# Kernel optimization log

Hardware: AMD Instinct MI355X
Metric: run time of the kernel (lower is better)

## Reference

```python
import jax, jax.numpy as jnp
import numpy as np

N_NODES = 50000
N_EDGES = 800000
HIDDEN = 128
IN_DIM = 128
OUT_DIM = 1
N_LAYERS = 4
N_GRAPHS = 32
LN_EPS = 1e-5


def setup_inputs() -> dict:
    key = jax.random.key(0)
    ks = jax.random.split(key, 12)
    s = 1.0 / np.sqrt(HIDDEN)
    inp = {
        "x": jax.random.normal(ks[0], (N_NODES, IN_DIM), dtype=jnp.float32),
        "edge_index": jax.random.randint(ks[1], (2, N_EDGES), 0, N_NODES, dtype=jnp.int64),
        "batch": jnp.sort(jax.random.randint(ks[2], (N_NODES,), 0, N_GRAPHS, dtype=jnp.int64)),
        "W_emb": jax.random.normal(ks[3], (HIDDEN, IN_DIM), dtype=jnp.float32) * s,
        "b_emb": jax.random.normal(ks[4], (HIDDEN,), dtype=jnp.float32) * s,
        "W_layers": jax.random.normal(ks[5], (N_LAYERS, HIDDEN, HIDDEN), dtype=jnp.float32) * s,
        "b_layers": jax.random.normal(ks[6], (N_LAYERS, HIDDEN), dtype=jnp.float32) * s,
        "ln_gamma": 1.0 + 0.02 * jax.random.normal(ks[7], (N_LAYERS, HIDDEN), dtype=jnp.float32),
        "ln_beta": 0.02 * jax.random.normal(ks[8], (N_LAYERS, HIDDEN), dtype=jnp.float32),
        "W_out": jax.random.normal(ks[9], (OUT_DIM, HIDDEN), dtype=jnp.float32) * s,
    }
    return inp


def _layer_norm(x, gamma, beta):
    mu = jnp.mean(x, axis=-1, keepdims=True)
    var = jnp.mean(jnp.square(x - mu), axis=-1, keepdims=True)
    return (x - mu) * jax.lax.rsqrt(var + LN_EPS) * gamma + beta


def reference(x, edge_index, batch, W_emb, b_emb, W_layers, b_layers, ln_gamma, ln_beta, W_out):
    n = x.shape[0]
    # add self-loops (PyG GCNConv default)
    loop = jnp.arange(n, dtype=edge_index.dtype)
    row = jnp.concatenate([edge_index[0], loop])  # source nodes
    col = jnp.concatenate([edge_index[1], loop])  # target nodes
    # symmetric normalization: deg over targets
    deg = jax.ops.segment_sum(jnp.ones_like(col, dtype=x.dtype), col, num_segments=n)
    dis = jnp.where(deg > 0, jax.lax.rsqrt(jnp.maximum(deg, 1.0)), 0.0)
    norm = dis[row] * dis[col]  # [E+N]

    h = x @ W_emb.T + b_emb  # embedding layer
    for i in range(N_LAYERS):
        t = h @ W_layers[i].T                      # [N, H] linear first
        msg = t[row] * norm[:, None]               # gather + scale  [E+N, H]
        agg = jax.ops.segment_sum(msg, col, num_segments=n) + b_layers[i]
        h = _layer_norm(h + jax.nn.relu(agg), ln_gamma[i], ln_beta[i])

    out = h @ W_out.T                              # [N, OUT_DIM]
    sums = jax.ops.segment_sum(out, batch, num_segments=N_GRAPHS)
    cnts = jax.ops.segment_sum(jnp.ones((n,), out.dtype), batch, num_segments=N_GRAPHS)
    return sums / jnp.maximum(cnts, 1.0)[:, None]  # [N_GRAPHS, OUT_DIM]
```

## Files before the change

### kernel.cpp

```cpp
#include <hip/hip_runtime.h>
#include <hip/hip_fp16.h>

#define NN 50000
#define NE 800000
#define NH 128
#define NG 32
#define NL 4
#define NB 196
#define WSLOT (NH * NH)

typedef __attribute__((ext_vector_type(8))) short bf16x8;
typedef __attribute__((ext_vector_type(4))) float f32x4;
typedef __attribute__((ext_vector_type(2))) float f32x2;

__device__ inline short f2bf(float x) {
  union { float f; unsigned u; } v;
  v.f = x;
  unsigned r = v.u + 0x7FFF + ((v.u >> 16) & 1);
  return (short)(r >> 16);
}
__device__ inline float bf2f(short s) {
  union { unsigned u; float f; } v;
  v.u = ((unsigned)(unsigned short)s) << 16;
  return v.f;
}

__device__ inline int block_exscan(int v) {
  __shared__ int wsum[4];
  int tid = threadIdx.x, wave = tid >> 6, lane = tid & 63;
  int x = v;
#pragma unroll
  for (int off = 1; off < 64; off <<= 1) {
    int y = __shfl_up(x, off, 64);
    if (lane >= off) x += y;
  }
  if (lane == 63) wsum[wave] = x;
  __syncthreads();
  int wp = 0;
  if (wave > 0) wp += wsum[0];
  if (wave > 1) wp += wsum[1];
  if (wave > 2) wp += wsum[2];
  return wp + x - v;
}

__global__ __launch_bounds__(256) void prep_swizzle(const float* __restrict__ W_emb,
                                                    const float* __restrict__ W_layers,
                                                    short* __restrict__ hi,
                                                    short* __restrict__ lo) {
  int i = blockIdx.x * 256 + threadIdx.x;
  if (i >= 5 * WSLOT) return;
  int slot = i >> 14, f = i & (WSLOT - 1);
  int j = f & 7, lane = (f >> 3) & 63, tt = (f >> 9) & 7, ks = f >> 12;
  int n = tt * 16 + (lane & 15);
  int k = ks * 32 + ((lane >> 4) & 3) * 8 + j;
  const float* W = slot ? (W_layers + (size_t)(slot - 1) * WSLOT) : W_emb;
  float x = W[n * NH + k];
  short hh = f2bf(x);
  hi[i] = hh;
  lo[i] = f2bf(x - bf2f(hh));
}

__global__ __launch_bounds__(256) void hist_kernel(const int* __restrict__ col,
                                                   int* __restrict__ cnt,
                                                   int* __restrict__ rank) {
  int e = blockIdx.x * 256 + threadIdx.x;
  if (e < NE) rank[e] = atomicAdd(&cnt[col[e]], 1);
}

__global__ __launch_bounds__(256) void scan1_kernel(const int* __restrict__ cnt,
                                                    int* __restrict__ bsum,
                                                    float* __restrict__ dis) {
  int i = blockIdx.x * 256 + threadIdx.x;
  int v = (i < NN) ? cnt[i] : 0;
  if (i < NN) dis[i] = rsqrtf((float)(v + 1));
  int lane = threadIdx.x & 63;
  int s = v;
#pragma unroll
  for (int off = 32; off; off >>= 1) s += __shfl_down(s, off, 64);
  __shared__ int ws[4];
  if (lane == 0) ws[threadIdx.x >> 6] = s;
  __syncthreads();
  if (threadIdx.x == 0) bsum[blockIdx.x] = ws[0] + ws[1] + ws[2] + ws[3];
}

__global__ __launch_bounds__(256) void scan2_kernel(const int* __restrict__ bsum,
                                                    int* __restrict__ ebsum) {
  int tid = threadIdx.x;
  int v = (tid < NB) ? bsum[tid] : 0;
  int ex = block_exscan(v);
  if (tid < NB) ebsum[tid] = ex;
}

__global__ __launch_bounds__(256) void scan3_kernel(const int* __restrict__ cnt,
                                                    const int* __restrict__ ebsum,
                                                    int* __restrict__ offs) {
  int i = blockIdx.x * 256 + threadIdx.x;
  int v = (i < NN) ? cnt[i] : 0;
  int ex = block_exscan(v);
  if (i < NN) offs[i] = ebsum[blockIdx.x] + ex;
}

__global__ __launch_bounds__(256) void fill_kernel(const int* __restrict__ row,
                                                   const int* __restrict__ col,
                                                   const int* __restrict__ rank,
                                                   const float* __restrict__ dis,
                                                   const int* __restrict__ offs,
                                                   int2* __restrict__ csr) {
  int e = blockIdx.x * 256 + threadIdx.x;
  if (e < NE) {
    int d = col[e];
    int s = row[e];
    int pos = offs[d] + rank[e];
    csr[pos] = make_int2(s, __float_as_int(dis[s] * dis[d]));
  }
}

template <bool EMB, bool LAST>
__global__ __launch_bounds__(512) void gemm_mfma(const float* __restrict__ Xf,
                                                 const __half* __restrict__ Xh,
                                                 const short* __restrict__ Whi,
                                                 const short* __restrict__ Wlo,
                                                 const float* __restrict__ bias,
                                                 const __half* __restrict__ hprev,
                                                 const float* __restrict__ gamma,
                                                 const float* __restrict__ beta,
                                                 const float* __restrict__ Wout,
                                                 __half* __restrict__ hnew,
                                                 unsigned char* __restrict__ h8,
                                                 float* __restrict__ nodeval) {
  __shared__ short Wh[WSLOT];
  __shared__ short Wl[WSLOT];
  int tid = threadIdx.x;
#pragma unroll
  for (int i = tid * 8; i < WSLOT; i += 512 * 8) {
    *(bf16x8*)&Wh[i] = *(const bf16x8*)(Whi + i);
    *(bf16x8*)&Wl[i] = *(const bf16x8*)(Wlo + i);
  }
  __syncthreads();

  int wave = tid >> 6, lane = tid & 63;
  int quad = lane >> 4, r16 = lane & 15;
  int m0 = blockIdx.x * 128 + wave * 16;
  if (m0 >= NN) return;
  int mA = m0 + r16;

  f32x4 acc[8];
#pragma unroll
  for (int t = 0; t < 8; ++t) acc[t] = (f32x4){0.f, 0.f, 0.f, 0.f};

#pragma unroll
  for (int ks = 0; ks < 4; ++ks) {
    int klane = ks * 32 + quad * 8;
    float af[8];
    if (EMB) {
      const float* xr = Xf + (size_t)mA * NH + klane;
      float4 a0 = *(const float4*)xr;
      float4 a1 = *(const float4*)(xr + 4);
      af[0] = a0.x; af[1] = a0.y; af[2] = a0.z; af[3] = a0.w;
      af[4] = a1.x; af[5] = a1.y; af[6] = a1.z; af[7] = a1.w;
    } else {
      const __half2* xr = (const __half2*)(Xh + (size_t)mA * NH + klane);
#pragma unroll
      for (int q = 0; q < 4; ++q) {
        float2 f = __half22float2(xr[q]);
        af[2 * q] = f.x;
        af[2 * q + 1] = f.y;
      }
    }
    bf16x8 xhi, xlo;
#pragma unroll
    for (int j = 0; j < 8; ++j) {
      short h = f2bf(af[j]);
      xhi[j] = h;
      xlo[j] = f2bf(af[j] - bf2f(h));
    }
#pragma unroll
    for (int t = 0; t < 8; ++t) {
      int fidx = ((ks * 8 + t) * 64 + lane) << 3;
      bf16x8 whi = *(const bf16x8*)&Wh[fidx];
      bf16x8 wlo = *(const bf16x8*)&Wl[fidx];
      acc[t] = __builtin_amdgcn_mfma_f32_16x16x32_bf16(whi, xhi, acc[t], 0, 0, 0);
      acc[t] = __builtin_amdgcn_mfma_f32_16x16x32_bf16(whi, xlo, acc[t], 0, 0, 0);
      acc[t] = __builtin_amdgcn_mfma_f32_16x16x32_bf16(wlo, xhi, acc[t], 0, 0, 0);
    }
  }

  int m = m0 + r16;
  int cb = quad * 4;
  if (EMB) {
#pragma unroll
    for (int t = 0; t < 8; ++t) {
      int ch = t * 16 + cb;
      float4 bb = *(const float4*)(bias + ch);
      float o0 = acc[t][0] + bb.x, o1 = acc[t][1] + bb.y;
      float o2 = acc[t][2] + bb.z, o3 = acc[t][3] + bb.w;
      __half2 p01 = __float22half2_rn(make_float2(o0, o1));
      __half2 p23 = __float22half2_rn(make_float2(o2, o3));
      *(uint2*)(hnew + (size_t)m * NH + ch) =
          make_uint2(*(unsigned*)&p01, *(unsigned*)&p23);
      int v = 0;
      v = __builtin_amdgcn_cvt_pk_fp8_f32(o0, o1, v, 0);
      v = __builtin_amdgcn_cvt_pk_fp8_f32(o2, o3, v, 1);
      ((unsigned*)(h8 + (size_t)m * NH))[t * 4 + quad] = (unsigned)v;
    }
  } else {
    float v[8][4];
    float s = 0.f, s2 = 0.f;
#pragma unroll
    for (int t = 0; t < 8; ++t) {
      int ch = t * 16 + cb;
      float4 bb = *(const float4*)(bias + ch);
      uint2 hp = *(const uint2*)(hprev + (size_t)m * NH + ch);
      float2 h01 = __half22float2(*(__half2*)&hp.x);
      float2 h23 = __half22float2(*(__half2*)&hp.y);
      float hv[4] = {h01.x, h01.y, h23.x, h23.y};
      float bb4[4] = {bb.x, bb.y, bb.z, bb.w};
#pragma unroll
      for (int r = 0; r < 4; ++r) {
        float z = fmaxf(acc[t][r] + bb4[r], 0.f);
        float val = hv[r] + z;
        v[t][r] = val;
        s += val;
        s2 += val * val;
      }
    }
    s += __shfl_xor(s, 16, 64);
    s += __shfl_xor(s, 32, 64);
    s2 += __shfl_xor(s2, 16, 64);
    s2 += __shfl_xor(s2, 32, 64);
    float mean = s * (1.f / 128.f);
    float var = fmaxf(s2 * (1.f / 128.f) - mean * mean, 0.f);
    float inv = rsqrtf(var + 1e-5f);
    float d = 0.f;
#pragma unroll
    for (int t = 0; t < 8; ++t) {
      int ch = t * 16 + cb;
      float4 gv = *(const float4*)(gamma + ch);
      float4 bt = *(const float4*)(beta + ch);
      float o0 = (v[t][0] - mean) * inv * gv.x + bt.x;
      float o1 = (v[t][1] - mean) * inv * gv.y + bt.y;
      float o2 = (v[t][2] - mean) * inv * gv.z + bt.z;
      float o3 = (v[t][3] - mean) * inv * gv.w + bt.w;
      __half2 p01 = __float22half2_rn(make_float2(o0, o1));
      __half2 p23 = __float22half2_rn(make_float2(o2, o3));
      *(uint2*)(hnew + (size_t)m * NH + ch) =
          make_uint2(*(unsigned*)&p01, *(unsigned*)&p23);
      if (!LAST) {
        int pv = 0;
        pv = __builtin_amdgcn_cvt_pk_fp8_f32(o0, o1, pv, 0);
        pv = __builtin_amdgcn_cvt_pk_fp8_f32(o2, o3, pv, 1);
        ((unsigned*)(h8 + (size_t)m * NH))[t * 4 + quad] = (unsigned)pv;
      } else {
        float4 wv = *(const float4*)(Wout + ch);
        d += o0 * wv.x + o1 * wv.y + o2 * wv.z + o3 * wv.w;
      }
    }
    if (LAST) {
      d += __shfl_xor(d, 16, 64);
      d += __shfl_xor(d, 32, 64);
      if (lane < 16) nodeval[m] = d;
    }
  }
}

__global__ __launch_bounds__(256) void aggregate_kernel(
    const unsigned char* __restrict__ h8, __half* __restrict__ agg,
    const float* __restrict__ dis, const int* __restrict__ offs,
    const int* __restrict__ cnt, const int2* __restrict__ csr) {
  int node = blockIdx.x * 4 + (threadIdx.x >> 6);
  int lane = threadIdx.x & 63;
  if (node >= NN) return;
  int hf = lane >> 5;
  int c32 = lane & 31;
  const unsigned* t32 = (const unsigned*)h8;
  float dii = dis[node];
  float sl = dii * dii;
  float4 a = make_float4(0.f, 0.f, 0.f, 0.f);
  if (hf == 0) {
    unsigned raw = t32[(size_t)node * 32 + c32];
    f32x2 lo2 = __builtin_amdgcn_cvt_pk_f32_fp8(raw, 0);
    f32x2 hi2 = __builtin_amdgcn_cvt_pk_f32_fp8(raw, 1);
    a.x = lo2.x * sl; a.y = lo2.y * sl; a.z = hi2.x * sl; a.w = hi2.y * sl;
  }
  int s0 = offs[node];
  int e = cnt[node];
  int j = 0;
  for (; j + 16 <= e; j += 16) {
    int2 p[8];
    unsigned raw[8];
#pragma unroll
    for (int u = 0; u < 8; ++u) p[u] = csr[s0 + j + 2 * u + hf];
#pragma unroll
    for (int u = 0; u < 8; ++u) raw[u] = t32[(size_t)p[u].x * 32 + c32];
#pragma unroll
    for (int u = 0; u < 8; ++u) {
      float w = __int_as_float(p[u].y);
      f32x2 lo2 = __builtin_amdgcn_cvt_pk_f32_fp8(raw[u], 0);
      f32x2 hi2 = __builtin_amdgcn_cvt_pk_f32_fp8(raw[u], 1);
      a.x += lo2.x * w; a.y += lo2.y * w; a.z += hi2.x * w; a.w += hi2.y * w;
    }
  }
  for (; j + 8 <= e; j += 8) {
    int2 p[4];
    unsigned raw[4];
#pragma unroll
    for (int u = 0; u < 4; ++u) p[u] = csr[s0 + j + 2 * u + hf];
#pragma unroll
    for (int u = 0; u < 4; ++u) raw[u] = t32[(size_t)p[u].x * 32 + c32];
#pragma unroll
    for (int u = 0; u < 4; ++u) {
      float w = __int_as_float(p[u].y);
      f32x2 lo2 = __builtin_amdgcn_cvt_pk_f32_fp8(raw[u], 0);
      f32x2 hi2 = __builtin_amdgcn_cvt_pk_f32_fp8(raw[u], 1);
      a.x += lo2.x * w; a.y += lo2.y * w; a.z += hi2.x * w; a.w += hi2.y * w;
    }
  }
  for (; j < e; j += 2) {
    int idx = j + hf;
    int2 p = (idx < e) ? csr[s0 + idx] : make_int2(node, 0);
    float w = __int_as_float(p.y);
    unsigned raw = t32[(size_t)p.x * 32 + c32];
    f32x2 lo2 = __builtin_amdgcn_cvt_pk_f32_fp8(raw, 0);
    f32x2 hi2 = __builtin_amdgcn_cvt_pk_f32_fp8(raw, 1);
    a.x += lo2.x * w; a.y += lo2.y * w; a.z += hi2.x * w; a.w += hi2.y * w;
  }
  a.x += __shfl_down(a.x, 32, 64);
  a.y += __shfl_down(a.y, 32, 64);
  a.z += __shfl_down(a.z, 32, 64);
  a.w += __shfl_down(a.w, 32, 64);
  if (lane < 32) {
    __half2 p01 = __float22half2_rn(make_float2(a.x, a.y));
    __half2 p23 = __float22half2_rn(make_float2(a.z, a.w));
    *(uint2*)(agg + (size_t)node * NH + (c32 << 2)) =
        make_uint2(*(unsigned*)&p01, *(unsigned*)&p23);
  }
}

__global__ __launch_bounds__(256) void reduce_pool_kernel(
    const float* __restrict__ nodeval, const int* __restrict__ batch,
    float* __restrict__ gsum, int* __restrict__ gcnt) {
  __shared__ float bins[NG];
  __shared__ int cbins[NG];
  int tid = threadIdx.x;
  if (tid < NG) {
    bins[tid] = 0.f;
    cbins[tid] = 0;
  }
  __syncthreads();
  int i = blockIdx.x * 256 + tid;
  if (i < NN) {
    int g = batch[i];
    atomicAdd(&bins[g], nodeval[i]);
    atomicAdd(&cbins[g], 1);
  }
  __syncthreads();
  if (tid < NG) {
    if (cbins[tid]) {
      atomicAdd(&gsum[tid], bins[tid]);
      atomicAdd(&gcnt[tid], cbins[tid]);
    }
  }
}

__global__ void finalize_kernel(const float* __restrict__ gsum,
                                const int* __restrict__ gcnt,
                                float* __restrict__ out) {
  int g = threadIdx.x;
  if (g < NG) out[g] = gsum[g] / fmaxf((float)gcnt[g], 1.0f);
}

extern "C" void kernel_launch(void* const* d_in, const int* in_sizes, int n_in,
                              void* d_out, int out_size, void* d_ws, size_t ws_size,
                              hipStream_t stream) {
  const float* x = (const float*)d_in[0];
  const int* eidx = (const int*)d_in[1];
  const int* batch = (const int*)d_in[2];
  const float* W_emb = (const float*)d_in[3];
  const float* b_emb = (const float*)d_in[4];
  const float* W_layers = (const float*)d_in[5];
  const float* b_layers = (const float*)d_in[6];
  const float* ln_gamma = (const float*)d_in[7];
  const float* ln_beta = (const float*)d_in[8];
  const float* W_out = (const float*)d_in[9];
  float* out = (float*)d_out;

  char* ws = (char*)d_ws;
  unsigned char* h8 = (unsigned char*)ws; ws += (size_t)NN * NH;
  __half* h = (__half*)ws;      ws += (size_t)NN * NH * 2;
  __half* agg = (__half*)ws;    ws += (size_t)NN * NH * 2;
  short* Whi = (short*)ws;      ws += (size_t)5 * WSLOT * 2;
  short* Wlo = (short*)ws;      ws += (size_t)5 * WSLOT * 2;
  float* dis = (float*)ws;      ws += (size_t)NN * 4;
  int2* csr = (int2*)ws;        ws += (size_t)NE * 8;
  int* rank = (int*)ws;         ws += (size_t)NE * 4;
  int* offs = (int*)ws;         ws += (size_t)NN * 4;
  float* nodeval = (float*)ws;  ws += (size_t)NN * 4;
  int* bsum = (int*)ws;         ws += (size_t)NB * 4;
  int* ebsum = (int*)ws;        ws += (size_t)NB * 4;
  char* zero_base = ws;
  int* cnt = (int*)ws;          ws += (size_t)NN * 4;
  float* gsum = (float*)ws;     ws += (size_t)NG * 4;
  int* gcnt = (int*)ws;         ws += (size_t)NG * 4;
  size_t zero_bytes = (size_t)(ws - zero_base);
  hipMemsetAsync(zero_base, 0, zero_bytes, stream);

  const int* erow = eidx;
  const int* ecol = eidx + NE;

  prep_swizzle<<<(5 * WSLOT + 255) / 256, 256, 0, stream>>>(W_emb, W_layers, Whi,
                                                            Wlo);
  hist_kernel<<<(NE + 255) / 256, 256, 0, stream>>>(ecol, cnt, rank);
  scan1_kernel<<<NB, 256, 0, stream>>>(cnt, bsum, dis);
  scan2_kernel<<<1, 256, 0, stream>>>(bsum, ebsum);
  scan3_kernel<<<NB, 256, 0, stream>>>(cnt, ebsum, offs);
  fill_kernel<<<(NE + 255) / 256, 256, 0, stream>>>(erow, ecol, rank, dis, offs,
                                                    csr);
  int gblk = (NN + 127) / 128;
  gemm_mfma<true, false><<<gblk, 512, 0, stream>>>(
      x, nullptr, Whi, Wlo, b_emb, nullptr, nullptr, nullptr, nullptr, h, h8,
      nullptr);
  for (int l = 0; l < NL; ++l) {
    aggregate_kernel<<<(NN + 3) / 4, 256, 0, stream>>>(h8, agg, dis, offs, cnt,
                                                       csr);
    const short* wh = Whi + (size_t)(l + 1) * WSLOT;
    const short* wl = Wlo + (size_t)(l + 1) * WSLOT;
    const float* bl = b_layers + (size_t)l * NH;
    const float* gl = ln_gamma + (size_t)l * NH;
    const float* be = ln_beta + (size_t)l * NH;
    if (l == NL - 1)
      gemm_mfma<false, true><<<gblk, 512, 0, stream>>>(
          nullptr, agg, wh, wl, bl, h, gl, be, W_out, h, h8, nodeval);
    else
      gemm_mfma<false, false><<<gblk, 512, 0, stream>>>(
          nullptr, agg, wh, wl, bl, h, gl, be, nullptr, h, h8, nullptr);
  }
  reduce_pool_kernel<<<(NN + 255) / 256, 256, 0, stream>>>(nodeval, batch, gsum,
                                                           gcnt);
  finalize_kernel<<<1, 64, 0, stream>>>(gsum, gcnt, out);
}
```

Before: 377.2 us.

## Split aggregation into two channel-half launches with four edge lanes per wavefront

The aggregation kernel now launches twice as many blocks. Each block handles one half of the 128 channels (16 lanes × 4 fp8) and processes four edges per iteration instead of two, with an extra shuffle reduction at the end. This raises parallelism and in-flight gathers per node. In exchange, every CSR entry is read twice and each gathered row access is only 64 bytes wide. Separately, the last layer's GEMM no longer writes the unused fp16 hidden state, which drops one dead global store.

```diff
diff --git a/kernel.cpp b/kernel.cpp
--- a/kernel.cpp
+++ b/kernel.cpp
@@ -8,6 +8,7 @@
 #define NL 4
 #define NB 196
 #define WSLOT (NH * NH)
+#define ABLK 12500
 
 typedef __attribute__((ext_vector_type(8))) short bf16x8;
 typedef __attribute__((ext_vector_type(4))) float f32x4;
@@ -241,11 +242,11 @@
       float o1 = (v[t][1] - mean) * inv * gv.y + bt.y;
       float o2 = (v[t][2] - mean) * inv * gv.z + bt.z;
       float o3 = (v[t][3] - mean) * inv * gv.w + bt.w;
-      __half2 p01 = __float22half2_rn(make_float2(o0, o1));
-      __half2 p23 = __float22half2_rn(make_float2(o2, o3));
-      *(uint2*)(hnew + (size_t)m * NH + ch) =
-          make_uint2(*(unsigned*)&p01, *(unsigned*)&p23);
       if (!LAST) {
+        __half2 p01 = __float22half2_rn(make_float2(o0, o1));
+        __half2 p23 = __float22half2_rn(make_float2(o2, o3));
+        *(uint2*)(hnew + (size_t)m * NH + ch) =
+            make_uint2(*(unsigned*)&p01, *(unsigned*)&p23);
         int pv = 0;
         pv = __builtin_amdgcn_cvt_pk_fp8_f32(o0, o1, pv, 0);
         pv = __builtin_amdgcn_cvt_pk_fp8_f32(o2, o3, pv, 1);
@@ -263,21 +264,24 @@
   }
 }
 
-__global__ __launch_bounds__(256) void aggregate_kernel(
+__global__ __launch_bounds__(256) void aggregate_half_kernel(
     const unsigned char* __restrict__ h8, __half* __restrict__ agg,
     const float* __restrict__ dis, const int* __restrict__ offs,
     const int* __restrict__ cnt, const int2* __restrict__ csr) {
-  int node = blockIdx.x * 4 + (threadIdx.x >> 6);
+  int half = blockIdx.x >= ABLK;
+  int blk = blockIdx.x - (half ? ABLK : 0);
+  int node = blk * 4 + (threadIdx.x >> 6);
   int lane = threadIdx.x & 63;
   if (node >= NN) return;
-  int hf = lane >> 5;
-  int c32 = lane & 31;
+  int ef = lane >> 4;
+  int c16 = lane & 15;
+  int hb = half * 16 + c16;
   const unsigned* t32 = (const unsigned*)h8;
   float dii = dis[node];
   float sl = dii * dii;
   float4 a = make_float4(0.f, 0.f, 0.f, 0.f);
-  if (hf == 0) {
-    unsigned raw = t32[(size_t)node * 32 + c32];
+  if (ef == 0) {
+    unsigned raw = t32[(size_t)node * 32 + hb];
     f32x2 lo2 = __builtin_amdgcn_cvt_pk_f32_fp8(raw, 0);
     f32x2 hi2 = __builtin_amdgcn_cvt_pk_f32_fp8(raw, 1);
     a.x = lo2.x * sl; a.y = lo2.y * sl; a.z = hi2.x * sl; a.w = hi2.y * sl;
@@ -286,27 +290,12 @@
   int e = cnt[node];
   int j = 0;
   for (; j + 16 <= e; j += 16) {
-    int2 p[8];
-    unsigned raw[8];
-#pragma unroll
-    for (int u = 0; u < 8; ++u) p[u] = csr[s0 + j + 2 * u + hf];
-#pragma unroll
-    for (int u = 0; u < 8; ++u) raw[u] = t32[(size_t)p[u].x * 32 + c32];
-#pragma unroll
-    for (int u = 0; u < 8; ++u) {
-      float w = __int_as_float(p[u].y);
-      f32x2 lo2 = __builtin_amdgcn_cvt_pk_f32_fp8(raw[u], 0);
-      f32x2 hi2 = __builtin_amdgcn_cvt_pk_f32_fp8(raw[u], 1);
-      a.x += lo2.x * w; a.y += lo2.y * w; a.z += hi2.x * w; a.w += hi2.y * w;
-    }
-  }
-  for (; j + 8 <= e; j += 8) {
     int2 p[4];
     unsigned raw[4];
 #pragma unroll
-    for (int u = 0; u < 4; ++u) p[u] = csr[s0 + j + 2 * u + hf];
-#pragma unroll
-    for (int u = 0; u < 4; ++u) raw[u] = t32[(size_t)p[u].x * 32 + c32];
+    for (int u = 0; u < 4; ++u) p[u] = csr[s0 + j + 4 * u + ef];
+#pragma unroll
+    for (int u = 0; u < 4; ++u) raw[u] = t32[(size_t)p[u].x * 32 + hb];
 #pragma unroll
     for (int u = 0; u < 4; ++u) {
       float w = __int_as_float(p[u].y);
@@ -315,11 +304,26 @@
       a.x += lo2.x * w; a.y += lo2.y * w; a.z += hi2.x * w; a.w += hi2.y * w;
     }
   }
-  for (; j < e; j += 2) {
-    int idx = j + hf;
+  for (; j + 8 <= e; j += 8) {
+    int2 p[2];
+    unsigned raw[2];
+#pragma unroll
+    for (int u = 0; u < 2; ++u) p[u] = csr[s0 + j + 4 * u + ef];
+#pragma unroll
+    for (int u = 0; u < 2; ++u) raw[u] = t32[(size_t)p[u].x * 32 + hb];
+#pragma unroll
+    for (int u = 0; u < 2; ++u) {
+      float w = __int_as_float(p[u].y);
+      f32x2 lo2 = __builtin_amdgcn_cvt_pk_f32_fp8(raw[u], 0);
+      f32x2 hi2 = __builtin_amdgcn_cvt_pk_f32_fp8(raw[u], 1);
+      a.x += lo2.x * w; a.y += lo2.y * w; a.z += hi2.x * w; a.w += hi2.y * w;
+    }
+  }
+  for (; j < e; j += 4) {
+    int idx = j + ef;
     int2 p = (idx < e) ? csr[s0 + idx] : make_int2(node, 0);
     float w = __int_as_float(p.y);
-    unsigned raw = t32[(size_t)p.x * 32 + c32];
+    unsigned raw = t32[(size_t)p.x * 32 + hb];
     f32x2 lo2 = __builtin_amdgcn_cvt_pk_f32_fp8(raw, 0);
     f32x2 hi2 = __builtin_amdgcn_cvt_pk_f32_fp8(raw, 1);
     a.x += lo2.x * w; a.y += lo2.y * w; a.z += hi2.x * w; a.w += hi2.y * w;
@@ -328,10 +332,14 @@
   a.y += __shfl_down(a.y, 32, 64);
   a.z += __shfl_down(a.z, 32, 64);
   a.w += __shfl_down(a.w, 32, 64);
-  if (lane < 32) {
+  a.x += __shfl_down(a.x, 16, 64);
+  a.y += __shfl_down(a.y, 16, 64);
+  a.z += __shfl_down(a.z, 16, 64);
+  a.w += __shfl_down(a.w, 16, 64);
+  if (lane < 16) {
     __half2 p01 = __float22half2_rn(make_float2(a.x, a.y));
     __half2 p23 = __float22half2_rn(make_float2(a.z, a.w));
-    *(uint2*)(agg + (size_t)node * NH + (c32 << 2)) =
+    *(uint2*)(agg + (size_t)node * NH + (hb << 2)) =
         make_uint2(*(unsigned*)&p01, *(unsigned*)&p23);
   }
 }
@@ -420,8 +428,8 @@
       x, nullptr, Whi, Wlo, b_emb, nullptr, nullptr, nullptr, nullptr, h, h8,
       nullptr);
   for (int l = 0; l < NL; ++l) {
-    aggregate_kernel<<<(NN + 3) / 4, 256, 0, stream>>>(h8, agg, dis, offs, cnt,
-                                                       csr);
+    aggregate_half_kernel<<<2 * ABLK, 256, 0, stream>>>(h8, agg, dis, offs, cnt,
+                                                        csr);
     const short* wh = Whi + (size_t)(l + 1) * WSLOT;
     const short* wl = Wlo + (size_t)(l + 1) * WSLOT;
     const float* bl = b_layers + (size_t)l * NH;
@@ -429,7 +437,7 @@
     const float* be = ln_beta + (size_t)l * NH;
     if (l == NL - 1)
       gemm_mfma<false, true><<<gblk, 512, 0, stream>>>(
-          nullptr, agg, wh, wl, bl, h, gl, be, W_out, h, h8, nodeval);
+          nullptr, agg, wh, wl, bl, h, gl, be, W_out, nullptr, nullptr, nodeval);
     else
       gemm_mfma<false, false><<<gblk, 512, 0, stream>>>(
           nullptr, agg, wh, wl, bl, h, gl, be, nullptr, h, h8, nullptr);
```

New measurement: 419.0 us. +11.1%, slower.

## Fuse neighbor aggregation with layer GEMM and LayerNorm via LDS staging

Applied to the files above, without the earlier changes.

Replaces the separate aggregate and per-layer GEMM kernels with one gcn_layer kernel. Each wave aggregates 16 nodes' fp8 neighbor features into a bf16 tile in shared memory, then runs MFMA, bias, ReLU, residual and LayerNorm on that tile, removing the fp16 agg round trip through global memory and one launch per layer. The layer GEMM also drops the hi/lo split-bf16 correction terms and uses a single bf16 product, and the fp8 feature buffer is double-buffered so gathers do not race with writes. Each wave now aggregates 16 nodes one after another, which may reduce memory-level parallelism in the gather, and the single bf16 product lowers accuracy.

```diff
diff --git a/kernel.cpp b/kernel.cpp
--- a/kernel.cpp
+++ b/kernel.cpp
@@ -8,6 +8,7 @@
 #define NL 4
 #define NB 196
 #define WSLOT (NH * NH)
+#define ROWSH 136
 
 typedef __attribute__((ext_vector_type(8))) short bf16x8;
 typedef __attribute__((ext_vector_type(4))) float f32x4;
@@ -115,19 +116,12 @@
   }
 }
 
-template <bool EMB, bool LAST>
-__global__ __launch_bounds__(512) void gemm_mfma(const float* __restrict__ Xf,
-                                                 const __half* __restrict__ Xh,
-                                                 const short* __restrict__ Whi,
-                                                 const short* __restrict__ Wlo,
-                                                 const float* __restrict__ bias,
-                                                 const __half* __restrict__ hprev,
-                                                 const float* __restrict__ gamma,
-                                                 const float* __restrict__ beta,
-                                                 const float* __restrict__ Wout,
-                                                 __half* __restrict__ hnew,
-                                                 unsigned char* __restrict__ h8,
-                                                 float* __restrict__ nodeval) {
+__global__ __launch_bounds__(512) void gemm_emb(const float* __restrict__ Xf,
+                                                const short* __restrict__ Whi,
+                                                const short* __restrict__ Wlo,
+                                                const float* __restrict__ bias,
+                                                __half* __restrict__ hnew,
+                                                unsigned char* __restrict__ h8) {
   __shared__ short Wh[WSLOT];
   __shared__ short Wl[WSLOT];
   int tid = threadIdx.x;
@@ -151,22 +145,10 @@
 #pragma unroll
   for (int ks = 0; ks < 4; ++ks) {
     int klane = ks * 32 + quad * 8;
-    float af[8];
-    if (EMB) {
-      const float* xr = Xf + (size_t)mA * NH + klane;
-      float4 a0 = *(const float4*)xr;
-      float4 a1 = *(const float4*)(xr + 4);
-      af[0] = a0.x; af[1] = a0.y; af[2] = a0.z; af[3] = a0.w;
-      af[4] = a1.x; af[5] = a1.y; af[6] = a1.z; af[7] = a1.w;
-    } else {
-      const __half2* xr = (const __half2*)(Xh + (size_t)mA * NH + klane);
-#pragma unroll
-      for (int q = 0; q < 4; ++q) {
-        float2 f = __half22float2(xr[q]);
-        af[2 * q] = f.x;
-        af[2 * q + 1] = f.y;
-      }
-    }
+    const float* xr = Xf + (size_t)mA * NH + klane;
+    float4 a0 = *(const float4*)xr;
+    float4 a1 = *(const float4*)(xr + 4);
+    float af[8] = {a0.x, a0.y, a0.z, a0.w, a1.x, a1.y, a1.z, a1.w};
     bf16x8 xhi, xlo;
 #pragma unroll
     for (int j = 0; j < 8; ++j) {
@@ -184,155 +166,188 @@
       acc[t] = __builtin_amdgcn_mfma_f32_16x16x32_bf16(wlo, xhi, acc[t], 0, 0, 0);
     }
   }
+  int m = m0 + r16;
+#pragma unroll
+  for (int t = 0; t < 8; ++t) {
+    int ch = t * 16 + quad * 4;
+    float4 bb = *(const float4*)(bias + ch);
+    float o0 = acc[t][0] + bb.x, o1 = acc[t][1] + bb.y;
+    float o2 = acc[t][2] + bb.z, o3 = acc[t][3] + bb.w;
+    __half2 p01 = __float22half2_rn(make_float2(o0, o1));
+    __half2 p23 = __float22half2_rn(make_float2(o2, o3));
+    *(uint2*)(hnew + (size_t)m * NH + ch) =
+        make_uint2(*(unsigned*)&p01, *(unsigned*)&p23);
+    int v = 0;
+    v = __builtin_amdgcn_cvt_pk_fp8_f32(o0, o1, v, 0);
+    v = __builtin_amdgcn_cvt_pk_fp8_f32(o2, o3, v, 1);
+    ((unsigned*)(h8 + (size_t)m * NH))[t * 4 + quad] = (unsigned)v;
+  }
+}
+
+template <bool LAST>
+__global__ __launch_bounds__(256) void gcn_layer(
+    const unsigned char* __restrict__ h8in, const short* __restrict__ Wfrag,
+    const float* __restrict__ dis, const int* __restrict__ offs,
+    const int* __restrict__ cnt, const int2* __restrict__ csr,
+    const float* __restrict__ bias, const float* __restrict__ gamma,
+    const float* __restrict__ beta, const float* __restrict__ Wout,
+    __half* __restrict__ h, unsigned char* __restrict__ h8out,
+    float* __restrict__ nodeval) {
+  __shared__ short Wh[WSLOT];
+  __shared__ short aggS[64 * ROWSH];
+  int tid = threadIdx.x;
+#pragma unroll
+  for (int i = tid * 8; i < WSLOT; i += 256 * 8)
+    *(bf16x8*)&Wh[i] = *(const bf16x8*)(Wfrag + i);
+  __syncthreads();
+
+  int wave = tid >> 6, lane = tid & 63;
+  int quad = lane >> 4, r16 = lane & 15;
+  int m0 = blockIdx.x * 64 + wave * 16;
+  if (m0 >= NN) return;
+
+  const unsigned* t32 = (const unsigned*)h8in;
+  int hf = lane >> 5;
+  int c32 = lane & 31;
+  short* myAgg = aggS + wave * 16 * ROWSH;
+  for (int i = 0; i < 16; ++i) {
+    int node = m0 + i;
+    float dii = dis[node];
+    float sl = dii * dii;
+    float4 a = make_float4(0.f, 0.f, 0.f, 0.f);
+    if (hf == 0) {
+      unsigned raw = t32[(size_t)node * 32 + c32];
+      f32x2 lo2 = __builtin_amdgcn_cvt_pk_f32_fp8(raw, 0);
+      f32x2 hi2 = __builtin_amdgcn_cvt_pk_f32_fp8(raw, 1);
+      a.x = lo2.x * sl; a.y = lo2.y * sl; a.z = hi2.x * sl; a.w = hi2.y * sl;
+    }
+    int s0 = offs[node];
+    int e = cnt[node];
+    int j = 0;
+    for (; j + 16 <= e; j += 16) {
+      int2 p[8];
+      unsigned raw[8];
+#pragma unroll
+      for (int u = 0; u < 8; ++u) p[u] = csr[s0 + j + 2 * u + hf];
+#pragma unroll
+      for (int u = 0; u < 8; ++u) raw[u] = t32[(size_t)p[u].x * 32 + c32];
+#pragma unroll
+      for (int u = 0; u < 8; ++u) {
+        float w = __int_as_float(p[u].y);
+        f32x2 lo2 = __builtin_amdgcn_cvt_pk_f32_fp8(raw[u], 0);
+        f32x2 hi2 = __builtin_amdgcn_cvt_pk_f32_fp8(raw[u], 1);
+        a.x += lo2.x * w; a.y += lo2.y * w; a.z += hi2.x * w; a.w += hi2.y * w;
+      }
+    }
+    for (; j + 4 <= e; j += 4) {
+      int2 p[2];
+      unsigned raw[2];
+#pragma unroll
+      for (int u = 0; u < 2; ++u) p[u] = csr[s0 + j + 2 * u + hf];
+#pragma unroll
+      for (int u = 0; u < 2; ++u) raw[u] = t32[(size_t)p[u].x * 32 + c32];
+#pragma unroll
+      for (int u = 0; u < 2; ++u) {
+        float w = __int_as_float(p[u].y);
+        f32x2 lo2 = __builtin_amdgcn_cvt_pk_f32_fp8(raw[u], 0);
+        f32x2 hi2 = __builtin_amdgcn_cvt_pk_f32_fp8(raw[u], 1);
+        a.x += lo2.x * w; a.y += lo2.y * w; a.z += hi2.x * w; a.w += hi2.y * w;
+      }
+    }
+    for (; j < e; j += 2) {
+      int idx = j + hf;
+      int2 p = (idx < e) ? csr[s0 + idx] : make_int2(node, 0);
+      float w = __int_as_float(p.y);
+      unsigned raw = t32[(size_t)p.x * 32 + c32];
+      f32x2 lo2 = __builtin_amdgcn_cvt_pk_f32_fp8(raw, 0);
+      f32x2 hi2 = __builtin_amdgcn_cvt_pk_f32_fp8(raw, 1);
+      a.x += lo2.x * w; a.y += lo2.y * w; a.z += hi2.x * w; a.w += hi2.y * w;
+    }
+    a.x += __shfl_down(a.x, 32, 64);
+    a.y += __shfl_down(a.y, 32, 64);
+    a.z += __shfl_down(a.z, 32, 64);
+    a.w += __shfl_down(a.w, 32, 64);
+    if (lane < 32) {
+      unsigned u0 = ((unsigned)(unsigned short)f2bf(a.y) << 16) |
+                    (unsigned short)f2bf(a.x);
+      unsigned u1 = ((unsigned)(unsigned short)f2bf(a.w) << 16) |
+                    (unsigned short)f2bf(a.z);
+      *(uint2*)&myAgg[i * ROWSH + c32 * 4] = make_uint2(u0, u1);
+    }
+  }
+
+  f32x4 acc[8];
+#pragma unroll
+  for (int t = 0; t < 8; ++t) acc[t] = (f32x4){0.f, 0.f, 0.f, 0.f};
+#pragma unroll
+  for (int ks = 0; ks < 4; ++ks) {
+    int klane = ks * 32 + quad * 8;
+    bf16x8 xb = *(const bf16x8*)&myAgg[r16 * ROWSH + klane];
+#pragma unroll
+    for (int t = 0; t < 8; ++t) {
+      int fidx = ((ks * 8 + t) * 64 + lane) << 3;
+      bf16x8 wb = *(const bf16x8*)&Wh[fidx];
+      acc[t] = __builtin_amdgcn_mfma_f32_16x16x32_bf16(wb, xb, acc[t], 0, 0, 0);
+    }
+  }
 
   int m = m0 + r16;
   int cb = quad * 4;
-  if (EMB) {
-#pragma unroll
-    for (int t = 0; t < 8; ++t) {
-      int ch = t * 16 + cb;
-      float4 bb = *(const float4*)(bias + ch);
-      float o0 = acc[t][0] + bb.x, o1 = acc[t][1] + bb.y;
-      float o2 = acc[t][2] + bb.z, o3 = acc[t][3] + bb.w;
+  float v[8][4];
+  float s = 0.f, s2 = 0.f;
+#pragma unroll
+  for (int t = 0; t < 8; ++t) {
+    int ch = t * 16 + cb;
+    float4 bb = *(const float4*)(bias + ch);
+    uint2 hp = *(const uint2*)(h + (size_t)m * NH + ch);
+    float2 h01 = __half22float2(*(__half2*)&hp.x);
+    float2 h23 = __half22float2(*(__half2*)&hp.y);
+    float hv[4] = {h01.x, h01.y, h23.x, h23.y};
+    float bb4[4] = {bb.x, bb.y, bb.z, bb.w};
+#pragma unroll
+    for (int r = 0; r < 4; ++r) {
+      float z = fmaxf(acc[t][r] + bb4[r], 0.f);
+      float val = hv[r] + z;
+      v[t][r] = val;
+      s += val;
+      s2 += val * val;
+    }
+  }
+  s += __shfl_xor(s, 16, 64);
+  s += __shfl_xor(s, 32, 64);
+  s2 += __shfl_xor(s2, 16, 64);
+  s2 += __shfl_xor(s2, 32, 64);
+  float mean = s * (1.f / 128.f);
+  float var = fmaxf(s2 * (1.f / 128.f) - mean * mean, 0.f);
+  float inv = rsqrtf(var + 1e-5f);
+  float d = 0.f;
+#pragma unroll
+  for (int t = 0; t < 8; ++t) {
+    int ch = t * 16 + cb;
+    float4 gv = *(const float4*)(gamma + ch);
+    float4 bt = *(const float4*)(beta + ch);
+    float o0 = (v[t][0] - mean) * inv * gv.x + bt.x;
+    float o1 = (v[t][1] - mean) * inv * gv.y + bt.y;
+    float o2 = (v[t][2] - mean) * inv * gv.z + bt.z;
+    float o3 = (v[t][3] - mean) * inv * gv.w + bt.w;
+    if (!LAST) {
       __half2 p01 = __float22half2_rn(make_float2(o0, o1));
       __half2 p23 = __float22half2_rn(make_float2(o2, o3));
-      *(uint2*)(hnew + (size_t)m * NH + ch) =
+      *(uint2*)(h + (size_t)m * NH + ch) =
           make_uint2(*(unsigned*)&p01, *(unsigned*)&p23);
-      int v = 0;
-      v = __builtin_amdgcn_cvt_pk_fp8_f32(o0, o1, v, 0);
-      v = __builtin_amdgcn_cvt_pk_fp8_f32(o2, o3, v, 1);
-      ((unsigned*)(h8 + (size_t)m * NH))[t * 4 + quad] = (unsigned)v;
-    }
-  } else {
-    float v[8][4];
-    float s = 0.f, s2 = 0.f;
-#pragma unroll
-    for (int t = 0; t < 8; ++t) {
-      int ch = t * 16 + cb;
-      float4 bb = *(const float4*)(bias + ch);
-      uint2 hp = *(const uint2*)(hprev + (size_t)m * NH + ch);
-      float2 h01 = __half22float2(*(__half2*)&hp.x);
-      float2 h23 = __half22float2(*(__half2*)&hp.y);
-      float hv[4] = {h01.x, h01.y, h23.x, h23.y};
-      float bb4[4] = {bb.x, bb.y, bb.z, bb.w};
-#pragma unroll
-      for (int r = 0; r < 4; ++r) {
-        float z = fmaxf(acc[t][r] + bb4[r], 0.f);
-        float val = hv[r] + z;
-        v[t][r] = val;
-        s += val;
-        s2 += val * val;
-      }
-    }
-    s += __shfl_xor(s, 16, 64);
-    s += __shfl_xor(s, 32, 64);
-    s2 += __shfl_xor(s2, 16, 64);
-    s2 += __shfl_xor(s2, 32, 64);
-    float mean = s * (1.f / 128.f);
-    float var = fmaxf(s2 * (1.f / 128.f) - mean * mean, 0.f);
-    float inv = rsqrtf(var + 1e-5f);
-    float d = 0.f;
-#pragma unroll
-    for (int t = 0; t < 8; ++t) {
-      int ch = t * 16 + cb;
-      float4 gv = *(const float4*)(gamma + ch);
-      float4 bt = *(const float4*)(beta + ch);
-      float o0 = (v[t][0] - mean) * inv * gv.x + bt.x;
-      float o1 = (v[t][1] - mean) * inv * gv.y + bt.y;
-      float o2 = (v[t][2] - mean) * inv * gv.z + bt.z;
-      float o3 = (v[t][3] - mean) * inv * gv.w + bt.w;
-      __half2 p01 = __float22half2_rn(make_float2(o0, o1));
-      __half2 p23 = __float22half2_rn(make_float2(o2, o3));
-      *(uint2*)(hnew + (size_t)m * NH + ch) =
-          make_uint2(*(unsigned*)&p01, *(unsigned*)&p23);
-      if (!LAST) {
-        int pv = 0;
-        pv = __builtin_amdgcn_cvt_pk_fp8_f32(o0, o1, pv, 0);
-        pv = __builtin_amdgcn_cvt_pk_fp8_f32(o2, o3, pv, 1);
-        ((unsigned*)(h8 + (size_t)m * NH))[t * 4 + quad] = (unsigned)pv;
-      } else {
-        float4 wv = *(const float4*)(Wout + ch);
-        d += o0 * wv.x + o1 * wv.y + o2 * wv.z + o3 * wv.w;
-      }
-    }
-    if (LAST) {
-      d += __shfl_xor(d, 16, 64);
-      d += __shfl_xor(d, 32, 64);
-      if (lane < 16) nodeval[m] = d;
-    }
-  }
-}
-
-__global__ __launch_bounds__(256) void aggregate_kernel(
-    const unsigned char* __restrict__ h8, __half* __restrict__ agg,
-    const float* __restrict__ dis, const int* __restrict__ offs,
-    const int* __restrict__ cnt, const int2* __restrict__ csr) {
-  int node = blockIdx.x * 4 + (threadIdx.x >> 6);
-  int lane = threadIdx.x & 63;
-  if (node >= NN) return;
-  int hf = lane >> 5;
-  int c32 = lane & 31;
-  const unsigned* t32 = (const unsigned*)h8;
-  float dii = dis[node];
-  float sl = dii * dii;
-  float4 a = make_float4(0.f, 0.f, 0.f, 0.f);
-  if (hf == 0) {
-    unsigned raw = t32[(size_t)node * 32 + c32];
-    f32x2 lo2 = __builtin_amdgcn_cvt_pk_f32_fp8(raw, 0);
-    f32x2 hi2 = __builtin_amdgcn_cvt_pk_f32_fp8(raw, 1);
-    a.x = lo2.x * sl; a.y = lo2.y * sl; a.z = hi2.x * sl; a.w = hi2.y * sl;
-  }
-  int s0 = offs[node];
-  int e = cnt[node];
-  int j = 0;
-  for (; j + 16 <= e; j += 16) {
-    int2 p[8];
-    unsigned raw[8];
-#pragma unroll
-    for (int u = 0; u < 8; ++u) p[u] = csr[s0 + j + 2 * u + hf];
-#pragma unroll
-    for (int u = 0; u < 8; ++u) raw[u] = t32[(size_t)p[u].x * 32 + c32];
-#pragma unroll
-    for (int u = 0; u < 8; ++u) {
-      float w = __int_as_float(p[u].y);
-      f32x2 lo2 = __builtin_amdgcn_cvt_pk_f32_fp8(raw[u], 0);
-      f32x2 hi2 = __builtin_amdgcn_cvt_pk_f32_fp8(raw[u], 1);
-      a.x += lo2.x * w; a.y += lo2.y * w; a.z += hi2.x * w; a.w += hi2.y * w;
-    }
-  }
-  for (; j + 8 <= e; j += 8) {
-    int2 p[4];
-    unsigned raw[4];
-#pragma unroll
-    for (int u = 0; u < 4; ++u) p[u] = csr[s0 + j + 2 * u + hf];
-#pragma unroll
-    for (int u = 0; u < 4; ++u) raw[u] = t32[(size_t)p[u].x * 32 + c32];
-#pragma unroll
-    for (int u = 0; u < 4; ++u) {
-      float w = __int_as_float(p[u].y);
-      f32x2 lo2 = __builtin_amdgcn_cvt_pk_f32_fp8(raw[u], 0);
-      f32x2 hi2 = __builtin_amdgcn_cvt_pk_f32_fp8(raw[u], 1);
-      a.x += lo2.x * w; a.y += lo2.y * w; a.z += hi2.x * w; a.w += hi2.y * w;
-    }
-  }
-  for (; j < e; j += 2) {
-    int idx = j + hf;
-    int2 p = (idx < e) ? csr[s0 + idx] : make_int2(node, 0);
-    float w = __int_as_float(p.y);
-    unsigned raw = t32[(size_t)p.x * 32 + c32];
-    f32x2 lo2 = __builtin_amdgcn_cvt_pk_f32_fp8(raw, 0);
-    f32x2 hi2 = __builtin_amdgcn_cvt_pk_f32_fp8(raw, 1);
-    a.x += lo2.x * w; a.y += lo2.y * w; a.z += hi2.x * w; a.w += hi2.y * w;
-  }
-  a.x += __shfl_down(a.x, 32, 64);
-  a.y += __shfl_down(a.y, 32, 64);
-  a.z += __shfl_down(a.z, 32, 64);
-  a.w += __shfl_down(a.w, 32, 64);
-  if (lane < 32) {
-    __half2 p01 = __float22half2_rn(make_float2(a.x, a.y));
-    __half2 p23 = __float22half2_rn(make_float2(a.z, a.w));
-    *(uint2*)(agg + (size_t)node * NH + (c32 << 2)) =
-        make_uint2(*(unsigned*)&p01, *(unsigned*)&p23);
+      int pv = 0;
+      pv = __builtin_amdgcn_cvt_pk_fp8_f32(o0, o1, pv, 0);
+      pv = __builtin_amdgcn_cvt_pk_fp8_f32(o2, o3, pv, 1);
+      ((unsigned*)(h8out + (size_t)m * NH))[t * 4 + quad] = (unsigned)pv;
+    } else {
+      float4 wv = *(const float4*)(Wout + ch);
+      d += o0 * wv.x + o1 * wv.y + o2 * wv.z + o3 * wv.w;
+    }
+  }
+  if (LAST) {
+    d += __shfl_xor(d, 16, 64);
+    d += __shfl_xor(d, 32, 64);
+    if (lane < 16) nodeval[m] = d;
   }
 }
 
@@ -385,9 +400,9 @@
   float* out = (float*)d_out;
 
   char* ws = (char*)d_ws;
-  unsigned char* h8 = (unsigned char*)ws; ws += (size_t)NN * NH;
+  unsigned char* h8a = (unsigned char*)ws; ws += (size_t)NN * NH;
+  unsigned char* h8b = (unsigned char*)ws; ws += (size_t)NN * NH;
   __half* h = (__half*)ws;      ws += (size_t)NN * NH * 2;
-  __half* agg = (__half*)ws;    ws += (size_t)NN * NH * 2;
   short* Whi = (short*)ws;      ws += (size_t)5 * WSLOT * 2;
   short* Wlo = (short*)ws;      ws += (size_t)5 * WSLOT * 2;
   float* dis = (float*)ws;      ws += (size_t)NN * 4;
@@ -415,24 +430,24 @@
   scan3_kernel<<<NB, 256, 0, stream>>>(cnt, ebsum, offs);
   fill_kernel<<<(NE + 255) / 256, 256, 0, stream>>>(erow, ecol, rank, dis, offs,
                                                     csr);
-  int gblk = (NN + 127) / 128;
-  gemm_mfma<true, false><<<gblk, 512, 0, stream>>>(
-      x, nullptr, Whi, Wlo, b_emb, nullptr, nullptr, nullptr, nullptr, h, h8,
-      nullptr);
+  gemm_emb<<<(NN + 127) / 128, 512, 0, stream>>>(x, Whi, Wlo, b_emb, h, h8a);
+  int lblk = (NN + 63) / 64;
+  unsigned char* h8bufs[2] = {h8a, h8b};
   for (int l = 0; l < NL; ++l) {
-    aggregate_kernel<<<(NN + 3) / 4, 256, 0, stream>>>(h8, agg, dis, offs, cnt,
-                                                       csr);
     const short* wh = Whi + (size_t)(l + 1) * WSLOT;
-    const short* wl = Wlo + (size_t)(l + 1) * WSLOT;
     const float* bl = b_layers + (size_t)l * NH;
     const float* gl = ln_gamma + (size_t)l * NH;
     const float* be = ln_beta + (size_t)l * NH;
+    unsigned char* src = h8bufs[l & 1];
+    unsigned char* dst = h8bufs[(l + 1) & 1];
     if (l == NL - 1)
-      gemm_mfma<false, true><<<gblk, 512, 0, stream>>>(
-          nullptr, agg, wh, wl, bl, h, gl, be, W_out, h, h8, nodeval);
+      gcn_layer<true><<<lblk, 256, 0, stream>>>(src, wh, dis, offs, cnt, csr, bl,
+                                                gl, be, W_out, h, nullptr,
+                                                nodeval);
     else
-      gemm_mfma<false, false><<<gblk, 512, 0, stream>>>(
-          nullptr, agg, wh, wl, bl, h, gl, be, nullptr, h, h8, nullptr);
+      gcn_layer<false><<<lblk, 256, 0, stream>>>(src, wh, dis, offs, cnt, csr,
+                                                 bl, gl, be, nullptr, h, dst,
+                                                 nullptr);
   }
   reduce_pool_kernel<<<(NN + 255) / 256, 256, 0, stream>>>(nodeval, batch, gsum,
                                                            gcnt);
```

After: 561.1 us. +48.8%, slower.
